# Performance work log

Hardware: AMD Instinct MI355X
Metric: run time of the kernel (lower is better)

## Reference

```python
import jax, jax.numpy as jnp
import numpy as np

B, S, E = 8, 2048, 2048
H, O, C = 8, 16, 16  # n_state_heads, state_head_order, chunk; E == H*O*C
EPS = 1e-5


def layer_norm(x, w):
    mu = jnp.mean(x, axis=-1, keepdims=True)
    var = jnp.mean(jnp.square(x - mu), axis=-1, keepdims=True)
    return (x - mu) * jax.lax.rsqrt(var + EPS) * w


def setup_inputs() -> dict:
    key = jax.random.key(0)
    ks = jax.random.split(key, 8)
    activations = jax.random.normal(ks[0], (B, S, E), dtype=jnp.float32)
    last_state = jnp.eye(O, dtype=jnp.float32) + 0.01 * jax.random.normal(ks[1], (B, H, O, O), dtype=jnp.float32)
    w_up = 0.01 / (np.sqrt(C) * np.sqrt(O)) * jax.random.normal(ks[2], (O, C), dtype=jnp.float32)
    w_down = 0.1536 / np.sqrt(12) * jax.random.normal(ks[3], (C, O), dtype=jnp.float32)
    ln1_w = jnp.ones((E,), dtype=jnp.float32)
    ln2_w = jnp.ones((E,), dtype=jnp.float32)
    mlp_w1 = 0.02 * jax.random.normal(ks[4], (4 * E, E), dtype=jnp.float32)
    mlp_w2 = 0.02 / np.sqrt(12) * jax.random.normal(ks[5], (E, 4 * E), dtype=jnp.float32)
    return {"activations": activations, "last_state": last_state, "ln1_w": ln1_w,
            "ln2_w": ln2_w, "w_up": w_up, "w_down": w_down, "mlp_w1": mlp_w1, "mlp_w2": mlp_w2}


def reference(activations, last_state, ln1_w, ln2_w, w_up, w_down, mlp_w1, mlp_w2):
    x = layer_norm(activations, ln1_w)                       # [B,S,E]
    x = x.reshape(B, S, H, O, C)
    # state_matrices_up (Linear C->O, no bias) + identity
    new_m = jnp.einsum('bshoc,pc->bshop', x, w_up) + jnp.eye(O, dtype=x.dtype)  # [B,S,H,O,O]
    full = jnp.concatenate([last_state[:, None], new_m], axis=1)                 # [B,S+1,H,O,O]
    # inclusive prefix matrix product: result[t] = M0 @ M1 @ ... @ Mt (earliest leftmost)
    scanned = jax.lax.associative_scan(
        lambda a, b: jnp.einsum('...ij,...jk->...ik', a, b), full, axis=1)
    states = scanned[:, 1:]                                  # [B,S,H,O,O]
    mru_out = jnp.einsum('bshop,cp->bshoc', states, w_down).reshape(B, S, E)
    act = activations + mru_out
    h = layer_norm(act, ln2_w)
    h = jax.nn.gelu(h @ mlp_w1.T, approximate=False) @ mlp_w2.T
    act = act + h
    new_state = states[-1]  # faithful to original: indexes batch dim -> [S,H,O,O]
    return act, new_state
```

## Files before the change

### kernel.cpp

```cpp
#include <hip/hip_runtime.h>
#include <hip/hip_bf16.h>

#define BB 8
#define SS 2048
#define EE 2048
#define HH 8
#define WCH 32
#define TCH 64

typedef __attribute__((ext_vector_type(4))) float f32x4;
typedef __attribute__((ext_vector_type(8))) short s16x8;
typedef __attribute__((ext_vector_type(4))) unsigned short u16x4;
typedef __attribute__((ext_vector_type(8))) unsigned short u16x8;

__device__ inline unsigned short f2bf(float x) {
  unsigned u = __float_as_uint(x);
  unsigned r = (u + 0x7fffu + ((u >> 16) & 1u)) >> 16;
  return (unsigned short)r;
}

__device__ inline void gl_lds16(const void* g, void* l) {
  __builtin_amdgcn_global_load_lds(
      (__attribute__((address_space(1))) void*)(void*)(size_t)(const char*)g,
      (__attribute__((address_space(3))) void*)l, 16, 0, 0);
}

__global__ __launch_bounds__(256) void cast_bf16(const float* __restrict__ in,
                                                 unsigned short* __restrict__ out,
                                                 long n) {
  long i = ((long)blockIdx.x * 256 + threadIdx.x) * 8;
  if (i >= n) return;
  f32x4 a = *(const f32x4*)(in + i);
  f32x4 b = *(const f32x4*)(in + i + 4);
  u16x8 r;
#pragma unroll
  for (int j = 0; j < 4; ++j) { r[j] = f2bf(a[j]); r[4 + j] = f2bf(b[j]); }
  *(u16x8*)(out + i) = r;
}

__global__ __launch_bounds__(256) void ln1_newm(const float* __restrict__ acts,
                                                const float* __restrict__ lnw,
                                                const float* __restrict__ wup,
                                                float* __restrict__ Ms) {
  const int row = blockIdx.x;
  const int b = row >> 11, s = row & 2047;
  __shared__ float xr[2048];
  __shared__ float wu[272];
  __shared__ float redA[4], redB[4];
  const int t = threadIdx.x, lane = t & 63, w = t >> 6;
  const float* xp = acts + (long)row * EE;
  f32x4 v0 = *(const f32x4*)(xp + t * 4);
  f32x4 v1 = *(const f32x4*)(xp + 1024 + t * 4);
  float sum = 0.f, ss = 0.f;
#pragma unroll
  for (int i = 0; i < 4; ++i) {
    sum += v0[i] + v1[i];
    ss += v0[i] * v0[i] + v1[i] * v1[i];
  }
#pragma unroll
  for (int off = 32; off > 0; off >>= 1) {
    sum += __shfl_down(sum, off, 64);
    ss += __shfl_down(ss, off, 64);
  }
  if (lane == 0) { redA[w] = sum; redB[w] = ss; }
  __syncthreads();
  const float stot = redA[0] + redA[1] + redA[2] + redA[3];
  const float sstot = redB[0] + redB[1] + redB[2] + redB[3];
  const float mu = stot * (1.f / 2048.f);
  const float var = sstot * (1.f / 2048.f) - mu * mu;
  const float rs = rsqrtf(var + 1e-5f);
  f32x4 g0 = *(const f32x4*)(lnw + t * 4);
  f32x4 g1 = *(const f32x4*)(lnw + 1024 + t * 4);
#pragma unroll
  for (int i = 0; i < 4; ++i) {
    xr[t * 4 + i] = (v0[i] - mu) * rs * g0[i];
    xr[1024 + t * 4 + i] = (v1[i] - mu) * rs * g1[i];
  }
  wu[(t >> 4) * 17 + (t & 15)] = wup[t];
  __syncthreads();
  const int h = t >> 5, idx = t & 31, o = idx >> 1, p0 = (idx & 1) * 8;
  float acc[8] = {0.f, 0.f, 0.f, 0.f, 0.f, 0.f, 0.f, 0.f};
  const int xb = h * 256 + o * 16;
#pragma unroll
  for (int c = 0; c < 16; ++c) {
    const float xa = xr[xb + c];
#pragma unroll
    for (int pp = 0; pp < 8; ++pp) acc[pp] += xa * wu[(p0 + pp) * 17 + c];
  }
  float* mp = Ms + (((long)(b * HH + h)) * SS + s) * 256 + o * 16;
#pragma unroll
  for (int pp = 0; pp < 8; ++pp) {
    const int p = p0 + pp;
    mp[p] = acc[pp] + ((p == o) ? 1.f : 0.f);
  }
}

__global__ __launch_bounds__(64) void chunk_prod(const float* __restrict__ Ms,
                                                 float* __restrict__ Qb) {
  const int task = blockIdx.x;
  const int bh = task >> 6, ch = task & 63;
  const float* Mbase = Ms + ((long)bh * SS + ch * WCH) * 256;
  __shared__ float Al[272], Ml[272];
  const int t = threadIdx.x, o = t >> 2, c4 = t & 3;
  f32x4 v = *(const f32x4*)(Mbase + t * 4);
#pragma unroll
  for (int i = 0; i < 4; ++i) Al[o * 17 + c4 * 4 + i] = v[i];
  for (int j = 1; j < WCH; ++j) {
    f32x4 mv = *(const f32x4*)(Mbase + (long)j * 256 + t * 4);
    __syncthreads();
#pragma unroll
    for (int i = 0; i < 4; ++i) Ml[o * 17 + c4 * 4 + i] = mv[i];
    __syncthreads();
    float nr[4] = {0.f, 0.f, 0.f, 0.f};
#pragma unroll
    for (int cc = 0; cc < 16; ++cc) {
      const float a = Al[o * 17 + cc];
#pragma unroll
      for (int i = 0; i < 4; ++i) nr[i] += a * Ml[cc * 17 + c4 * 4 + i];
    }
    __syncthreads();
#pragma unroll
    for (int i = 0; i < 4; ++i) Al[o * 17 + c4 * 4 + i] = nr[i];
  }
  f32x4 q;
#pragma unroll
  for (int i = 0; i < 4; ++i) q[i] = Al[o * 17 + c4 * 4 + i];
  *(f32x4*)(Qb + (long)task * 256 + t * 4) = q;
}

__global__ __launch_bounds__(64) void chunk_scan(const float* __restrict__ last,
                                                 const float* __restrict__ Qb,
                                                 float* __restrict__ Rb) {
  const int bh = blockIdx.x;
  const int t = threadIdx.x, o = t >> 2, c4 = t & 3;
  __shared__ float Al[272], Ml[272];
  f32x4 v = *(const f32x4*)(last + (long)bh * 256 + t * 4);
#pragma unroll
  for (int i = 0; i < 4; ++i) Al[o * 17 + c4 * 4 + i] = v[i];
  *(f32x4*)(Rb + (long)bh * TCH * 256 + t * 4) = v;
  for (int c = 0; c < TCH - 1; ++c) {
    f32x4 q = *(const f32x4*)(Qb + ((long)bh * TCH + c) * 256 + t * 4);
    __syncthreads();
#pragma unroll
    for (int i = 0; i < 4; ++i) Ml[o * 17 + c4 * 4 + i] = q[i];
    __syncthreads();
    float nr[4] = {0.f, 0.f, 0.f, 0.f};
#pragma unroll
    for (int cc = 0; cc < 16; ++cc) {
      const float a = Al[o * 17 + cc];
#pragma unroll
      for (int i = 0; i < 4; ++i) nr[i] += a * Ml[cc * 17 + c4 * 4 + i];
    }
    __syncthreads();
#pragma unroll
    for (int i = 0; i < 4; ++i) Al[o * 17 + c4 * 4 + i] = nr[i];
    f32x4 w;
#pragma unroll
    for (int i = 0; i < 4; ++i) w[i] = nr[i];
    *(f32x4*)(Rb + ((long)bh * TCH + c + 1) * 256 + t * 4) = w;
  }
}

__global__ __launch_bounds__(64) void scan_apply(const float* __restrict__ Ms,
                                                 const float* __restrict__ Rb,
                                                 const float* __restrict__ acts,
                                                 const float* __restrict__ wdown,
                                                 float* __restrict__ out) {
  const int task = blockIdx.x;
  const int bh = task >> 6, ch = task & 63;
  const int b = bh >> 3, h = bh & 7;
  const int t = threadIdx.x, o = t >> 2, c4 = t & 3;
  __shared__ float Al[272], Ml[272], Wd[272];
  f32x4 r0 = *(const f32x4*)(Rb + (long)task * 256 + t * 4);
#pragma unroll
  for (int i = 0; i < 4; ++i) Al[o * 17 + c4 * 4 + i] = r0[i];
  f32x4 wv = *(const f32x4*)(wdown + t * 4);
#pragma unroll
  for (int i = 0; i < 4; ++i) Wd[o * 17 + c4 * 4 + i] = wv[i];
  for (int j = 0; j < WCH; ++j) {
    const int s = ch * WCH + j;
    f32x4 mv = *(const f32x4*)(Ms + ((long)bh * SS + s) * 256 + t * 4);
    __syncthreads();
#pragma unroll
    for (int i = 0; i < 4; ++i) Ml[o * 17 + c4 * 4 + i] = mv[i];
    __syncthreads();
    float nr[4] = {0.f, 0.f, 0.f, 0.f};
#pragma unroll
    for (int cc = 0; cc < 16; ++cc) {
      const float a = Al[o * 17 + cc];
#pragma unroll
      for (int i = 0; i < 4; ++i) nr[i] += a * Ml[cc * 17 + c4 * 4 + i];
    }
    __syncthreads();
#pragma unroll
    for (int i = 0; i < 4; ++i) Al[o * 17 + c4 * 4 + i] = nr[i];
    __syncthreads();
    float o2[4] = {0.f, 0.f, 0.f, 0.f};
#pragma unroll
    for (int p = 0; p < 16; ++p) {
      const float pr = Al[o * 17 + p];
#pragma unroll
      for (int i = 0; i < 4; ++i) o2[i] += pr * Wd[(c4 * 4 + i) * 17 + p];
    }
    const long e = ((long)(b * SS + s)) * EE + h * 256 + t * 4;
    f32x4 av = *(const f32x4*)(acts + e);
    f32x4 res;
#pragma unroll
    for (int i = 0; i < 4; ++i) res[i] = av[i] + o2[i];
    *(f32x4*)(out + e) = res;
    if (b == BB - 1) {
      f32x4 st;
#pragma unroll
      for (int i = 0; i < 4; ++i) st[i] = nr[i];
      *(f32x4*)(out + (long)BB * SS * EE + ((long)s * HH + h) * 256 + t * 4) = st;
    }
  }
}

__global__ __launch_bounds__(256) void ln2_cast(const float* __restrict__ act1,
                                                const float* __restrict__ lnw,
                                                unsigned short* __restrict__ xbf) {
  const int row = blockIdx.x;
  __shared__ float redA[4], redB[4];
  const int t = threadIdx.x, lane = t & 63, w = t >> 6;
  const float* xp = act1 + (long)row * EE;
  f32x4 v0 = *(const f32x4*)(xp + t * 4);
  f32x4 v1 = *(const f32x4*)(xp + 1024 + t * 4);
  float sum = 0.f, ss = 0.f;
#pragma unroll
  for (int i = 0; i < 4; ++i) {
    sum += v0[i] + v1[i];
    ss += v0[i] * v0[i] + v1[i] * v1[i];
  }
#pragma unroll
  for (int off = 32; off > 0; off >>= 1) {
    sum += __shfl_down(sum, off, 64);
    ss += __shfl_down(ss, off, 64);
  }
  if (lane == 0) { redA[w] = sum; redB[w] = ss; }
  __syncthreads();
  const float stot = redA[0] + redA[1] + redA[2] + redA[3];
  const float sstot = redB[0] + redB[1] + redB[2] + redB[3];
  const float mu = stot * (1.f / 2048.f);
  const float var = sstot * (1.f / 2048.f) - mu * mu;
  const float rs = rsqrtf(var + 1e-5f);
  f32x4 g0 = *(const f32x4*)(lnw + t * 4);
  f32x4 g1 = *(const f32x4*)(lnw + 1024 + t * 4);
  u16x4 o0, o1;
#pragma unroll
  for (int i = 0; i < 4; ++i) {
    o0[i] = f2bf((v0[i] - mu) * rs * g0[i]);
    o1[i] = f2bf((v1[i] - mu) * rs * g1[i]);
  }
  *(u16x4*)(xbf + (long)row * EE + t * 4) = o0;
  *(u16x4*)(xbf + (long)row * EE + 1024 + t * 4) = o1;
}

template <int EPI>
__global__ __launch_bounds__(256) void gemm_bt(const short* __restrict__ A,
                                               const short* __restrict__ Bt,
                                               void* __restrict__ C,
                                               int M, int N, int K) {
  __shared__ short As[8192];
  __shared__ short Bs[8192];
  const int tid = threadIdx.x;
  const int lane = tid & 63;
  const int m0 = blockIdx.y * 128;
  const int n0 = blockIdx.x * 128;
  const int wm = (tid >> 7) * 64;
  const int wn = ((tid >> 6) & 1) * 64;
  const int r = lane & 15, kq = lane >> 4;

  f32x4 acc[4][4];
#pragma unroll
  for (int i = 0; i < 4; ++i)
#pragma unroll
    for (int j = 0; j < 4; ++j) acc[i][j] = (f32x4){0.f, 0.f, 0.f, 0.f};

  for (int k0 = 0; k0 < K; k0 += 64) {
    __syncthreads();
#pragma unroll
    for (int i = 0; i < 4; ++i) {
      const int chunk = i * 256 + tid;
      const int row = chunk >> 3;
      const int cg = (chunk & 7) ^ (row & 7);
      gl_lds16(A + (long)(m0 + row) * K + k0 + cg * 8, &As[chunk * 8]);
    }
#pragma unroll
    for (int i = 0; i < 4; ++i) {
      const int chunk = i * 256 + tid;
      const int row = chunk >> 3;
      const int cg = (chunk & 7) ^ (row & 7);
      gl_lds16(Bt + (long)(n0 + row) * K + k0 + cg * 8, &Bs[chunk * 8]);
    }
    __syncthreads();
#pragma unroll
    for (int ks = 0; ks < 2; ++ks) {
      s16x8 af[4], bfr[4];
#pragma unroll
      for (int i = 0; i < 4; ++i) {
        const int rowA = wm + i * 16 + r;
        const int ca = (ks * 4 + kq) ^ (rowA & 7);
        af[i] = *(const s16x8*)&As[rowA * 64 + ca * 8];
        const int rowB = wn + i * 16 + r;
        const int cb = (ks * 4 + kq) ^ (rowB & 7);
        bfr[i] = *(const s16x8*)&Bs[rowB * 64 + cb * 8];
      }
#pragma unroll
      for (int i = 0; i < 4; ++i)
#pragma unroll
        for (int j = 0; j < 4; ++j)
          acc[i][j] = __builtin_amdgcn_mfma_f32_16x16x32_bf16(af[i], bfr[j],
                                                              acc[i][j], 0, 0, 0);
    }
  }
  const int q = lane >> 4;
#pragma unroll
  for (int i = 0; i < 4; ++i) {
#pragma unroll
    for (int j = 0; j < 4; ++j) {
      const int col = n0 + wn + j * 16 + r;
#pragma unroll
      for (int rr = 0; rr < 4; ++rr) {
        const int rowm = m0 + wm + i * 16 + q * 4 + rr;
        const float v = acc[i][j][rr];
        if (EPI == 0) {
          const float g = 0.5f * v * (1.0f + erff(v * 0.70710678118654752f));
          ((unsigned short*)C)[(long)rowm * N + col] = f2bf(g);
        } else {
          float* p = (float*)C + (long)rowm * N + col;
          *p += v;
        }
      }
    }
  }
}

extern "C" void kernel_launch(void* const* d_in, const int* in_sizes, int n_in,
                              void* d_out, int out_size, void* d_ws, size_t ws_size,
                              hipStream_t stream) {
  const float* acts = (const float*)d_in[0];
  const float* last = (const float*)d_in[1];
  const float* ln1w = (const float*)d_in[2];
  const float* ln2w = (const float*)d_in[3];
  const float* wup = (const float*)d_in[4];
  const float* wdn = (const float*)d_in[5];
  const float* w1 = (const float*)d_in[6];
  const float* w2 = (const float*)d_in[7];
  float* out = (float*)d_out;

  char* ws = (char*)d_ws;
  unsigned short* xbf = (unsigned short*)ws;
  unsigned short* w1b = (unsigned short*)(ws + 67108864);
  unsigned short* w2b = (unsigned short*)(ws + 67108864 + 33554432);
  char* X = ws + 134217728;
  float* Ms = (float*)X;
  float* Qb = (float*)(X + 134217728);
  float* Rb = (float*)(X + 134217728 + 4194304);
  unsigned short* h1 = (unsigned short*)X;

  cast_bf16<<<8192, 256, 0, stream>>>(w1, w1b, (long)8192 * 2048);
  cast_bf16<<<8192, 256, 0, stream>>>(w2, w2b, (long)8192 * 2048);
  ln1_newm<<<BB * SS, 256, 0, stream>>>(acts, ln1w, wup, Ms);
  chunk_prod<<<BB * HH * TCH, 64, 0, stream>>>(Ms, Qb);
  chunk_scan<<<BB * HH, 64, 0, stream>>>(last, Qb, Rb);
  scan_apply<<<BB * HH * TCH, 64, 0, stream>>>(Ms, Rb, acts, wdn, out);
  ln2_cast<<<BB * SS, 256, 0, stream>>>(out, ln2w, xbf);
  dim3 g1(8192 / 128, 16384 / 128);
  gemm_bt<0><<<g1, 256, 0, stream>>>((const short*)xbf, (const short*)w1b,
                                     (void*)h1, 16384, 8192, 2048);
  dim3 g2(2048 / 128, 16384 / 128);
  gemm_bt<1><<<g2, 256, 0, stream>>>((const short*)h1, (const short*)w2b,
                                     (void*)out, 16384, 2048, 8192);
}
```

Measured before the change: 1.630 ms.

## Replace MLP GEMMs with 256x256 double-buffered 8-wave pipelined MFMA kernel

Replaces the 128x128 single-buffered GEMM with a 256x256 tile kernel using 8 waves, double-buffered LDS, and staged global-to-LDS loads interleaved between four MFMA phases with setprio and barriers. Adds an XCD-aware block swizzle for L2 locality. The aim is to hide global load latency behind MFMA work and raise arithmetic intensity per tile. The cost is 128KB of LDS per block, which limits occupancy, plus more register pressure from 32 accumulators per thread.

```diff
diff --git a/kernel.cpp b/kernel.cpp
--- a/kernel.cpp
+++ b/kernel.cpp
@@ -256,84 +256,177 @@
   *(u16x4*)(xbf + (long)row * EE + 1024 + t * 4) = o1;
 }
 
+#define MFMA16 __builtin_amdgcn_mfma_f32_16x16x32_bf16
+#define SBAR() __builtin_amdgcn_s_barrier()
+#define SPRIO(x) __builtin_amdgcn_s_setprio(x)
+
 template <int EPI>
-__global__ __launch_bounds__(256) void gemm_bt(const short* __restrict__ A,
-                                               const short* __restrict__ Bt,
-                                               void* __restrict__ C,
-                                               int M, int N, int K) {
-  __shared__ short As[8192];
-  __shared__ short Bs[8192];
+__global__ __launch_bounds__(512, 2) void gemm8p(const short* __restrict__ A,
+                                                 const short* __restrict__ Bt,
+                                                 void* __restrict__ C,
+                                                 int M, int N, int K) {
+  __shared__ short lds[65536];
   const int tid = threadIdx.x;
   const int lane = tid & 63;
-  const int m0 = blockIdx.y * 128;
-  const int n0 = blockIdx.x * 128;
-  const int wm = (tid >> 7) * 64;
-  const int wn = ((tid >> 6) & 1) * 64;
+  const int wid = tid >> 6;
+  const int wm = wid >> 2, wn = wid & 3;
   const int r = lane & 15, kq = lane >> 4;
 
-  f32x4 acc[4][4];
-#pragma unroll
-  for (int i = 0; i < 4; ++i)
+  const int nx = gridDim.x;
+  const int orig = blockIdx.y * nx + blockIdx.x;
+  const int nwg = nx * gridDim.y;
+  const int swz = (orig & 7) * (nwg >> 3) + (orig >> 3);
+  const int by = swz / nx, bx = swz - by * nx;
+  const long m0 = (long)by * 256, n0 = (long)bx * 256;
+
+  const int NT = K >> 6;
+
+  f32x4 acc[8][4];
+#pragma unroll
+  for (int i = 0; i < 8; ++i)
 #pragma unroll
     for (int j = 0; j < 4; ++j) acc[i][j] = (f32x4){0.f, 0.f, 0.f, 0.f};
 
-  for (int k0 = 0; k0 < K; k0 += 64) {
-    __syncthreads();
+  long srcA[4], srcB[4];
+  int dst16[4];
+#pragma unroll
+  for (int j = 0; j < 4; ++j) {
+    const int c = tid + 512 * j;
+    const int row = c >> 3;
+    const int kc = (c & 7) ^ (row & 7);
+    srcA[j] = (m0 + row) * (long)K + kc * 8;
+    srcB[j] = (n0 + row) * (long)K + kc * 8;
+    dst16[j] = c * 8;
+  }
+#define STAGE_A(t2) { const int _b = (((t2) & 1) << 15); const int _k0 = (t2) << 6; \
+  _Pragma("unroll") for (int _j = 0; _j < 4; ++_j) \
+    gl_lds16(A + srcA[_j] + _k0, &lds[_b + dst16[_j]]); }
+#define STAGE_B(t2) { const int _b = 16384 + (((t2) & 1) << 15); const int _k0 = (t2) << 6; \
+  _Pragma("unroll") for (int _j = 0; _j < 4; ++_j) \
+    gl_lds16(Bt + srcB[_j] + _k0, &lds[_b + dst16[_j]]); }
+
+  int offA[8], offB[4];
+#pragma unroll
+  for (int i = 0; i < 8; ++i) offA[i] = (wm * 128 + i * 16 + r) * 64;
+#pragma unroll
+  for (int j = 0; j < 4; ++j) offB[j] = (wn * 64 + j * 16 + r) * 64;
+  const int c0 = (kq ^ (r & 7)) * 8;
+  const int c1 = ((4 + kq) ^ (r & 7)) * 8;
+
+  STAGE_A(0);
+  STAGE_B(0);
+  if (NT > 1) {
+    STAGE_A(1);
+    asm volatile("s_waitcnt vmcnt(4)" ::: "memory");
+  } else {
+    asm volatile("s_waitcnt vmcnt(0)" ::: "memory");
+  }
+  SBAR();
+
+  s16x8 af[4][2], bf[2][2];
+
+  for (int t = 0; t < NT; ++t) {
+    const int bA = (t & 1) << 15;
+    const int bB = 16384 + ((t & 1) << 15);
 #pragma unroll
     for (int i = 0; i < 4; ++i) {
-      const int chunk = i * 256 + tid;
-      const int row = chunk >> 3;
-      const int cg = (chunk & 7) ^ (row & 7);
-      gl_lds16(A + (long)(m0 + row) * K + k0 + cg * 8, &As[chunk * 8]);
-    }
+      af[i][0] = *(const s16x8*)&lds[bA + offA[i] + c0];
+      af[i][1] = *(const s16x8*)&lds[bA + offA[i] + c1];
+    }
+#pragma unroll
+    for (int j = 0; j < 2; ++j) {
+      bf[j][0] = *(const s16x8*)&lds[bB + offB[j] + c0];
+      bf[j][1] = *(const s16x8*)&lds[bB + offB[j] + c1];
+    }
+    SBAR();
+    SPRIO(1);
+#pragma unroll
+    for (int i = 0; i < 4; ++i)
+#pragma unroll
+      for (int j = 0; j < 2; ++j) {
+        acc[i][j] = MFMA16(af[i][0], bf[j][0], acc[i][j], 0, 0, 0);
+        acc[i][j] = MFMA16(af[i][1], bf[j][1], acc[i][j], 0, 0, 0);
+      }
+    SPRIO(0);
+    SBAR();
+#pragma unroll
+    for (int j = 0; j < 2; ++j) {
+      bf[j][0] = *(const s16x8*)&lds[bB + offB[2 + j] + c0];
+      bf[j][1] = *(const s16x8*)&lds[bB + offB[2 + j] + c1];
+    }
+    if (t + 1 < NT) STAGE_B(t + 1);
+    SBAR();
+    SPRIO(1);
+#pragma unroll
+    for (int i = 0; i < 4; ++i)
+#pragma unroll
+      for (int j = 0; j < 2; ++j) {
+        acc[i][2 + j] = MFMA16(af[i][0], bf[j][0], acc[i][2 + j], 0, 0, 0);
+        acc[i][2 + j] = MFMA16(af[i][1], bf[j][1], acc[i][2 + j], 0, 0, 0);
+      }
+    SPRIO(0);
+    SBAR();
 #pragma unroll
     for (int i = 0; i < 4; ++i) {
-      const int chunk = i * 256 + tid;
-      const int row = chunk >> 3;
-      const int cg = (chunk & 7) ^ (row & 7);
-      gl_lds16(Bt + (long)(n0 + row) * K + k0 + cg * 8, &Bs[chunk * 8]);
-    }
-    __syncthreads();
-#pragma unroll
-    for (int ks = 0; ks < 2; ++ks) {
-      s16x8 af[4], bfr[4];
-#pragma unroll
-      for (int i = 0; i < 4; ++i) {
-        const int rowA = wm + i * 16 + r;
-        const int ca = (ks * 4 + kq) ^ (rowA & 7);
-        af[i] = *(const s16x8*)&As[rowA * 64 + ca * 8];
-        const int rowB = wn + i * 16 + r;
-        const int cb = (ks * 4 + kq) ^ (rowB & 7);
-        bfr[i] = *(const s16x8*)&Bs[rowB * 64 + cb * 8];
+      af[i][0] = *(const s16x8*)&lds[bA + offA[4 + i] + c0];
+      af[i][1] = *(const s16x8*)&lds[bA + offA[4 + i] + c1];
+    }
+    SBAR();
+    SPRIO(1);
+#pragma unroll
+    for (int i = 0; i < 4; ++i)
+#pragma unroll
+      for (int j = 0; j < 2; ++j) {
+        acc[4 + i][2 + j] = MFMA16(af[i][0], bf[j][0], acc[4 + i][2 + j], 0, 0, 0);
+        acc[4 + i][2 + j] = MFMA16(af[i][1], bf[j][1], acc[4 + i][2 + j], 0, 0, 0);
       }
-#pragma unroll
-      for (int i = 0; i < 4; ++i)
-#pragma unroll
-        for (int j = 0; j < 4; ++j)
-          acc[i][j] = __builtin_amdgcn_mfma_f32_16x16x32_bf16(af[i], bfr[j],
-                                                              acc[i][j], 0, 0, 0);
-    }
-  }
-  const int q = lane >> 4;
-#pragma unroll
-  for (int i = 0; i < 4; ++i) {
+    SPRIO(0);
+    SBAR();
+#pragma unroll
+    for (int j = 0; j < 2; ++j) {
+      bf[j][0] = *(const s16x8*)&lds[bB + offB[j] + c0];
+      bf[j][1] = *(const s16x8*)&lds[bB + offB[j] + c1];
+    }
+    if (t + 2 < NT) STAGE_A(t + 2);
+    SBAR();
+    SPRIO(1);
+#pragma unroll
+    for (int i = 0; i < 4; ++i)
+#pragma unroll
+      for (int j = 0; j < 2; ++j) {
+        acc[4 + i][j] = MFMA16(af[i][0], bf[j][0], acc[4 + i][j], 0, 0, 0);
+        acc[4 + i][j] = MFMA16(af[i][1], bf[j][1], acc[4 + i][j], 0, 0, 0);
+      }
+    SPRIO(0);
+    if (t + 2 < NT) {
+      asm volatile("s_waitcnt vmcnt(4)" ::: "memory");
+    } else if (t + 1 < NT) {
+      asm volatile("s_waitcnt vmcnt(0)" ::: "memory");
+    }
+    SBAR();
+  }
+
+#pragma unroll
+  for (int i = 0; i < 8; ++i) {
 #pragma unroll
     for (int j = 0; j < 4; ++j) {
-      const int col = n0 + wn + j * 16 + r;
+      const long col = n0 + wn * 64 + j * 16 + r;
 #pragma unroll
       for (int rr = 0; rr < 4; ++rr) {
-        const int rowm = m0 + wm + i * 16 + q * 4 + rr;
+        const long rowm = m0 + wm * 128 + i * 16 + kq * 4 + rr;
         const float v = acc[i][j][rr];
         if (EPI == 0) {
           const float g = 0.5f * v * (1.0f + erff(v * 0.70710678118654752f));
-          ((unsigned short*)C)[(long)rowm * N + col] = f2bf(g);
+          ((unsigned short*)C)[rowm * N + col] = f2bf(g);
         } else {
-          float* p = (float*)C + (long)rowm * N + col;
+          float* p = (float*)C + rowm * N + col;
           *p += v;
         }
       }
     }
   }
+#undef STAGE_A
+#undef STAGE_B
 }
 
 extern "C" void kernel_launch(void* const* d_in, const int* in_sizes, int n_in,
@@ -366,10 +459,10 @@
   chunk_scan<<<BB * HH, 64, 0, stream>>>(last, Qb, Rb);
   scan_apply<<<BB * HH * TCH, 64, 0, stream>>>(Ms, Rb, acts, wdn, out);
   ln2_cast<<<BB * SS, 256, 0, stream>>>(out, ln2w, xbf);
-  dim3 g1(8192 / 128, 16384 / 128);
-  gemm_bt<0><<<g1, 256, 0, stream>>>((const short*)xbf, (const short*)w1b,
-                                     (void*)h1, 16384, 8192, 2048);
-  dim3 g2(2048 / 128, 16384 / 128);
-  gemm_bt<1><<<g2, 256, 0, stream>>>((const short*)h1, (const short*)w2b,
-                                     (void*)out, 16384, 2048, 8192);
-}
+  dim3 g1(8192 / 256, 16384 / 256);
+  gemm8p<0><<<g1, 512, 0, stream>>>((const short*)xbf, (const short*)w1b,
+                                    (void*)h1, 16384, 8192, 2048);
+  dim3 g2(2048 / 256, 16384 / 256);
+  gemm8p<1><<<g2, 512, 0, stream>>>((const short*)h1, (const short*)w2b,
+                                    (void*)out, 16384, 2048, 8192);
+}
```

Result: faster. 1.509 ms (-7.4%).

## Replace MLP GEMM with 256x256 eight-wave double-buffered pipelined kernel

Applied to the files above, without the earlier changes.

Replaces the simple 128x128 single-buffered bf16 GEMM with a 256x256-tile, 512-thread kernel. It double-buffers LDS with async global-to-LDS loads interleaved between MFMA quadrants, using s_setprio, explicit waitcnt and barriers. It also adds an XCD-aware block swizzle for L2 locality. The aim is to hide global load latency, raise arithmetic intensity per tile, and improve cache reuse for the two large MLP matmuls, at the cost of 128KB LDS per block and fragile hand-scheduled synchronization.

```diff
diff --git a/kernel.cpp b/kernel.cpp
--- a/kernel.cpp
+++ b/kernel.cpp
@@ -256,84 +256,159 @@
   *(u16x4*)(xbf + (long)row * EE + 1024 + t * 4) = o1;
 }
 
+#define MFMA16 __builtin_amdgcn_mfma_f32_16x16x32_bf16
+#define SBAR() __builtin_amdgcn_s_barrier()
+#define SPRIO(x) __builtin_amdgcn_s_setprio(x)
+
 template <int EPI>
-__global__ __launch_bounds__(256) void gemm_bt(const short* __restrict__ A,
-                                               const short* __restrict__ Bt,
-                                               void* __restrict__ C,
-                                               int M, int N, int K) {
-  __shared__ short As[8192];
-  __shared__ short Bs[8192];
+__global__ __launch_bounds__(512, 2) void gemm8p(const short* __restrict__ A,
+                                                 const short* __restrict__ Bt,
+                                                 void* __restrict__ C,
+                                                 int M, int N, int K) {
+  __shared__ short lds[65536];
   const int tid = threadIdx.x;
   const int lane = tid & 63;
-  const int m0 = blockIdx.y * 128;
-  const int n0 = blockIdx.x * 128;
-  const int wm = (tid >> 7) * 64;
-  const int wn = ((tid >> 6) & 1) * 64;
+  const int wid = tid >> 6;
+  const int wm = wid >> 2, wn = wid & 3;
   const int r = lane & 15, kq = lane >> 4;
 
-  f32x4 acc[4][4];
-#pragma unroll
-  for (int i = 0; i < 4; ++i)
+  const int nx = gridDim.x;
+  const int orig = blockIdx.y * nx + blockIdx.x;
+  const int nwg = nx * gridDim.y;
+  const int swz = (orig & 7) * (nwg >> 3) + (orig >> 3);
+  const int by = swz / nx, bx = swz - by * nx;
+  const long m0 = (long)by * 256, n0 = (long)bx * 256;
+
+  const int NT = K >> 6;
+
+  f32x4 acc[8][4];
+#pragma unroll
+  for (int i = 0; i < 8; ++i)
 #pragma unroll
     for (int j = 0; j < 4; ++j) acc[i][j] = (f32x4){0.f, 0.f, 0.f, 0.f};
 
-  for (int k0 = 0; k0 < K; k0 += 64) {
-    __syncthreads();
-#pragma unroll
-    for (int i = 0; i < 4; ++i) {
-      const int chunk = i * 256 + tid;
-      const int row = chunk >> 3;
-      const int cg = (chunk & 7) ^ (row & 7);
-      gl_lds16(A + (long)(m0 + row) * K + k0 + cg * 8, &As[chunk * 8]);
-    }
-#pragma unroll
-    for (int i = 0; i < 4; ++i) {
-      const int chunk = i * 256 + tid;
-      const int row = chunk >> 3;
-      const int cg = (chunk & 7) ^ (row & 7);
-      gl_lds16(Bt + (long)(n0 + row) * K + k0 + cg * 8, &Bs[chunk * 8]);
-    }
-    __syncthreads();
-#pragma unroll
-    for (int ks = 0; ks < 2; ++ks) {
-      s16x8 af[4], bfr[4];
-#pragma unroll
-      for (int i = 0; i < 4; ++i) {
-        const int rowA = wm + i * 16 + r;
-        const int ca = (ks * 4 + kq) ^ (rowA & 7);
-        af[i] = *(const s16x8*)&As[rowA * 64 + ca * 8];
-        const int rowB = wn + i * 16 + r;
-        const int cb = (ks * 4 + kq) ^ (rowB & 7);
-        bfr[i] = *(const s16x8*)&Bs[rowB * 64 + cb * 8];
-      }
-#pragma unroll
-      for (int i = 0; i < 4; ++i)
-#pragma unroll
-        for (int j = 0; j < 4; ++j)
-          acc[i][j] = __builtin_amdgcn_mfma_f32_16x16x32_bf16(af[i], bfr[j],
-                                                              acc[i][j], 0, 0, 0);
-    }
-  }
-  const int q = lane >> 4;
-#pragma unroll
-  for (int i = 0; i < 4; ++i) {
+  long sA0[2], sB0[2];
+  int dst[2];
+#pragma unroll
+  for (int j = 0; j < 2; ++j) {
+    const int c = tid + 512 * j;
+    const int row = c >> 3;
+    const int kc = (c & 7) ^ (row & 7);
+    sA0[j] = (m0 + row) * (long)K + kc * 8;
+    sB0[j] = (n0 + row) * (long)K + kc * 8;
+    dst[j] = c * 8;
+  }
+  const long hK = 128 * (long)K;
+
+#define STG_A(t2, h) { const int _u = (((t2) & 1) * 2 + (h)) * 8192; \
+  const long _o = (long)((t2) << 6) + (h) * hK; \
+  _Pragma("unroll") for (int _j = 0; _j < 2; ++_j) \
+    gl_lds16(A + sA0[_j] + _o, &lds[_u + dst[_j]]); }
+#define STG_B(t2, h) { const int _u = 32768 + (((t2) & 1) * 2 + (h)) * 8192; \
+  const long _o = (long)((t2) << 6) + (h) * hK; \
+  _Pragma("unroll") for (int _j = 0; _j < 2; ++_j) \
+    gl_lds16(Bt + sB0[_j] + _o, &lds[_u + dst[_j]]); }
+
+  int offA[4], offB[2];
+#pragma unroll
+  for (int i = 0; i < 4; ++i) offA[i] = (wm * 64 + i * 16 + r) * 64;
+#pragma unroll
+  for (int j = 0; j < 2; ++j) offB[j] = (wn * 32 + j * 16 + r) * 64;
+  const int c0 = (kq ^ (r & 7)) * 8;
+  const int c1 = ((4 + kq) ^ (r & 7)) * 8;
+
+  s16x8 af[4][2], bf[2][2];
+
+#define RD_A(h, pb) { _Pragma("unroll") for (int _i = 0; _i < 4; ++_i) { \
+    const int _ba = ((pb) + (h)) * 8192 + offA[_i]; \
+    af[_i][0] = *(const s16x8*)&lds[_ba + c0]; \
+    af[_i][1] = *(const s16x8*)&lds[_ba + c1]; } }
+#define RD_B(h, pb) { _Pragma("unroll") for (int _j = 0; _j < 2; ++_j) { \
+    const int _bb = 32768 + ((pb) + (h)) * 8192 + offB[_j]; \
+    bf[_j][0] = *(const s16x8*)&lds[_bb + c0]; \
+    bf[_j][1] = *(const s16x8*)&lds[_bb + c1]; } }
+#define MFMA_Q(I0, J0) { _Pragma("unroll") for (int _i = 0; _i < 4; ++_i) \
+  _Pragma("unroll") for (int _j = 0; _j < 2; ++_j) { \
+    acc[(I0) + _i][(J0) + _j] = MFMA16(af[_i][0], bf[_j][0], acc[(I0) + _i][(J0) + _j], 0, 0, 0); \
+    acc[(I0) + _i][(J0) + _j] = MFMA16(af[_i][1], bf[_j][1], acc[(I0) + _i][(J0) + _j], 0, 0, 0); } }
+
+  STG_A(0, 0); STG_A(0, 1); STG_B(0, 0); STG_B(0, 1);
+  STG_A(1, 0); STG_B(1, 1);
+  asm volatile("s_waitcnt vmcnt(4)" ::: "memory");
+  SBAR();
+
+  for (int t = 0; t < NT; t += 2) {
+    const bool s2 = (t + 2) < NT, s3 = (t + 3) < NT;
+    RD_A(0, 0); RD_B(0, 0);
+    STG_A(t + 1, 1);
+    asm volatile("s_waitcnt lgkmcnt(8)" ::: "memory");
+    SBAR();
+    SPRIO(1); MFMA_Q(0, 0); SPRIO(0);
+    SBAR();
+    RD_B(1, 0);
+    STG_B(t + 1, 0);
+    SBAR();
+    SPRIO(1); MFMA_Q(0, 2); SPRIO(0);
+    SBAR();
+    RD_A(1, 0);
+    if (s2) STG_A(t + 2, 0);
+    SBAR();
+    SPRIO(1); MFMA_Q(4, 2); SPRIO(0);
+    SBAR();
+    RD_B(0, 0);
+    if (s2) STG_B(t + 2, 1);
+    SBAR();
+    SPRIO(1); MFMA_Q(4, 0); SPRIO(0);
+    asm volatile("s_waitcnt vmcnt(4)" ::: "memory");
+    SBAR();
+    RD_A(0, 2); RD_B(0, 2);
+    if (s2) STG_A(t + 2, 1);
+    asm volatile("s_waitcnt lgkmcnt(8)" ::: "memory");
+    SBAR();
+    SPRIO(1); MFMA_Q(0, 0); SPRIO(0);
+    SBAR();
+    RD_B(1, 2);
+    if (s2) STG_B(t + 2, 0);
+    SBAR();
+    SPRIO(1); MFMA_Q(0, 2); SPRIO(0);
+    SBAR();
+    RD_A(1, 2);
+    if (s3) STG_A(t + 3, 0);
+    SBAR();
+    SPRIO(1); MFMA_Q(4, 2); SPRIO(0);
+    SBAR();
+    RD_B(0, 2);
+    if (s3) STG_B(t + 3, 1);
+    SBAR();
+    SPRIO(1); MFMA_Q(4, 0); SPRIO(0);
+    asm volatile("s_waitcnt vmcnt(4)" ::: "memory");
+    SBAR();
+  }
+
+#pragma unroll
+  for (int i = 0; i < 8; ++i) {
 #pragma unroll
     for (int j = 0; j < 4; ++j) {
-      const int col = n0 + wn + j * 16 + r;
+      const long col = n0 + (j >> 1) * 128 + wn * 32 + (j & 1) * 16 + r;
 #pragma unroll
       for (int rr = 0; rr < 4; ++rr) {
-        const int rowm = m0 + wm + i * 16 + q * 4 + rr;
+        const long rowm = m0 + (i >> 2) * 128 + wm * 64 + (i & 3) * 16 + kq * 4 + rr;
         const float v = acc[i][j][rr];
         if (EPI == 0) {
           const float g = 0.5f * v * (1.0f + erff(v * 0.70710678118654752f));
-          ((unsigned short*)C)[(long)rowm * N + col] = f2bf(g);
+          ((unsigned short*)C)[rowm * N + col] = f2bf(g);
         } else {
-          float* p = (float*)C + (long)rowm * N + col;
+          float* p = (float*)C + rowm * N + col;
           *p += v;
         }
       }
     }
   }
+#undef STG_A
+#undef STG_B
+#undef RD_A
+#undef RD_B
+#undef MFMA_Q
 }
 
 extern "C" void kernel_launch(void* const* d_in, const int* in_sizes, int n_in,
@@ -366,10 +441,10 @@
   chunk_scan<<<BB * HH, 64, 0, stream>>>(last, Qb, Rb);
   scan_apply<<<BB * HH * TCH, 64, 0, stream>>>(Ms, Rb, acts, wdn, out);
   ln2_cast<<<BB * SS, 256, 0, stream>>>(out, ln2w, xbf);
-  dim3 g1(8192 / 128, 16384 / 128);
-  gemm_bt<0><<<g1, 256, 0, stream>>>((const short*)xbf, (const short*)w1b,
-                                     (void*)h1, 16384, 8192, 2048);
-  dim3 g2(2048 / 128, 16384 / 128);
-  gemm_bt<1><<<g2, 256, 0, stream>>>((const short*)h1, (const short*)w2b,
-                                     (void*)out, 16384, 2048, 8192);
-}
+  dim3 g1(8192 / 256, 16384 / 256);
+  gemm8p<0><<<g1, 512, 0, stream>>>((const short*)xbf, (const short*)w1b,
+                                    (void*)h1, 16384, 8192, 2048);
+  dim3 g2(2048 / 256, 16384 / 256);
+  gemm8p<1><<<g2, 512, 0, stream>>>((const short*)h1, (const short*)w2b,
+                                    (void*)out, 16384, 2048, 8192);
+}
```

After: 1.426 ms. 1.14x faster.

## Stage GEMM epilogue through LDS for vectorized stores and swizzle block order

Applied to the files above, without the earlier changes.

The GEMM epilogue now writes accumulator fragments into LDS, then reads them back as 16-byte rows so global stores (bf16 GELU output) and read-modify-writes (fp32 residual add) are coalesced and vectorized instead of scattered scalar accesses. Workgroup IDs are also remapped so consecutive blocks are spread across XCDs in groups of eight, aiming for better L2 locality. This adds an extra barrier and LDS round trip per tile.

```diff
diff --git a/kernel.cpp b/kernel.cpp
--- a/kernel.cpp
+++ b/kernel.cpp
@@ -256,20 +256,28 @@
   *(u16x4*)(xbf + (long)row * EE + 1024 + t * 4) = o1;
 }
 
+#define MFMA16 __builtin_amdgcn_mfma_f32_16x16x32_bf16
+
 template <int EPI>
-__global__ __launch_bounds__(256) void gemm_bt(const short* __restrict__ A,
+__global__ __launch_bounds__(256) void gemm128(const short* __restrict__ A,
                                                const short* __restrict__ Bt,
                                                void* __restrict__ C,
                                                int M, int N, int K) {
-  __shared__ short As[8192];
-  __shared__ short Bs[8192];
+  __shared__ __align__(16) short As[8192];
+  __shared__ __align__(16) short Bs[8192];
   const int tid = threadIdx.x;
   const int lane = tid & 63;
-  const int m0 = blockIdx.y * 128;
-  const int n0 = blockIdx.x * 128;
-  const int wm = (tid >> 7) * 64;
-  const int wn = ((tid >> 6) & 1) * 64;
+  const int wid = tid >> 6;
   const int r = lane & 15, kq = lane >> 4;
+
+  const int nx = gridDim.x;
+  const int orig = blockIdx.y * nx + blockIdx.x;
+  const int nwg = nx * gridDim.y;
+  const int swz = (orig & 7) * (nwg >> 3) + (orig >> 3);
+  const int by = swz / nx, bx = swz - by * nx;
+  const long m0 = (long)by * 128, n0 = (long)bx * 128;
+  const int wm = (wid >> 1) * 64;
+  const int wn = (wid & 1) * 64;
 
   f32x4 acc[4][4];
 #pragma unroll
@@ -310,27 +318,63 @@
       for (int i = 0; i < 4; ++i)
 #pragma unroll
         for (int j = 0; j < 4; ++j)
-          acc[i][j] = __builtin_amdgcn_mfma_f32_16x16x32_bf16(af[i], bfr[j],
-                                                              acc[i][j], 0, 0, 0);
-    }
-  }
-  const int q = lane >> 4;
-#pragma unroll
-  for (int i = 0; i < 4; ++i) {
-#pragma unroll
-    for (int j = 0; j < 4; ++j) {
-      const int col = n0 + wn + j * 16 + r;
-#pragma unroll
-      for (int rr = 0; rr < 4; ++rr) {
-        const int rowm = m0 + wm + i * 16 + q * 4 + rr;
-        const float v = acc[i][j][rr];
-        if (EPI == 0) {
+          acc[i][j] = MFMA16(af[i], bfr[j], acc[i][j], 0, 0, 0);
+    }
+  }
+  __syncthreads();
+
+  short* lds0 = (wid < 2) ? As : Bs;
+  if (EPI == 0) {
+    unsigned short* Wl = (unsigned short*)lds0 + (wid & 1) * 4096;
+#pragma unroll
+    for (int i = 0; i < 4; ++i)
+#pragma unroll
+      for (int j = 0; j < 4; ++j)
+#pragma unroll
+        for (int rr = 0; rr < 4; ++rr) {
+          const int rs = i * 16 + kq * 4 + rr;
+          const int cs = (j & 1) * 16 + r;
+          const float v = acc[i][j][rr];
           const float g = 0.5f * v * (1.0f + erff(v * 0.70710678118654752f));
-          ((unsigned short*)C)[(long)rowm * N + col] = f2bf(g);
-        } else {
-          float* p = (float*)C + (long)rowm * N + col;
-          *p += v;
+          Wl[(j >> 1) * 2048 + rs * 32 + cs] = f2bf(g);
         }
+    unsigned short* Cb = (unsigned short*)C;
+#pragma unroll
+    for (int s = 0; s < 2; ++s) {
+      const long cg = n0 + wn + s * 32 + (lane & 3) * 8;
+#pragma unroll
+      for (int it = 0; it < 4; ++it) {
+        const int rs = it * 16 + (lane >> 2);
+        u16x8 v = *(const u16x8*)&Wl[s * 2048 + rs * 32 + (lane & 3) * 8];
+        const long rg = m0 + wm + rs;
+        *(u16x8*)&Cb[rg * N + cg] = v;
+      }
+    }
+  } else {
+    float* Wl = (float*)lds0 + (wid & 1) * 2048;
+    float* Cf = (float*)C;
+#pragma unroll
+    for (int s = 0; s < 2; ++s) {
+#pragma unroll
+      for (int i = 0; i < 4; ++i)
+#pragma unroll
+        for (int j = 0; j < 2; ++j)
+#pragma unroll
+          for (int rr = 0; rr < 4; ++rr) {
+            const int rs = i * 16 + kq * 4 + rr;
+            Wl[rs * 32 + j * 16 + r] = acc[i][s * 2 + j][rr];
+          }
+      const long cg = n0 + wn + s * 32 + (lane & 7) * 4;
+#pragma unroll
+      for (int it = 0; it < 8; ++it) {
+        const int rs = it * 8 + (lane >> 3);
+        f32x4 v = *(const f32x4*)&Wl[rs * 32 + (lane & 7) * 4];
+        const long rg = m0 + wm + rs;
+        float* p = &Cf[rg * N + cg];
+        f32x4 o = *(const f32x4*)p;
+#pragma unroll
+        for (int e = 0; e < 4; ++e) o[e] += v[e];
+        *(f32x4*)p = o;
       }
     }
   }
@@ -367,9 +411,9 @@
   scan_apply<<<BB * HH * TCH, 64, 0, stream>>>(Ms, Rb, acts, wdn, out);
   ln2_cast<<<BB * SS, 256, 0, stream>>>(out, ln2w, xbf);
   dim3 g1(8192 / 128, 16384 / 128);
-  gemm_bt<0><<<g1, 256, 0, stream>>>((const short*)xbf, (const short*)w1b,
+  gemm128<0><<<g1, 256, 0, stream>>>((const short*)xbf, (const short*)w1b,
                                      (void*)h1, 16384, 8192, 2048);
   dim3 g2(2048 / 128, 16384 / 128);
-  gemm_bt<1><<<g2, 256, 0, stream>>>((const short*)h1, (const short*)w2b,
+  gemm128<1><<<g2, 256, 0, stream>>>((const short*)h1, (const short*)w2b,
                                      (void*)out, 16384, 2048, 8192);
 }
```

Result: slower. 1.690 ms (+3.7%).
